# Performance work log

Hardware: AMD Instinct MI355X
Metric: run time of the kernel (lower is better)

## Reference

```python
import jax, jax.numpy as jnp
import numpy as np

# torchvision Grayscale luminance weights
_GRAY_W = np.array([0.2989, 0.587, 0.114], dtype=np.float32)

# Unnormalized DCT-II matrix as used by torch_dct.dct(norm=None):
#   X_k = 2 * sum_n x_n * cos(pi * (2n+1) * k / (2N)),  N = 8
_N = 8
_n = np.arange(_N)
_DCT_M = (2.0 * np.cos(np.pi * (2.0 * _n[None, :] + 1.0) * _n[:, None] / (2.0 * _N))).astype(np.float32)  # [k, n]


def setup_inputs() -> dict:
    key = jax.random.key(0)
    # (B, C, T, H, W) video batch in [0, 1)
    x = jax.random.uniform(key, (8, 3, 32, 256, 256), dtype=jnp.float32)
    return {"x": x}


def reference(x):
    B, C, T, H, W = x.shape
    # permute (B, C, T, H, W) -> (B, T, C, H, W)
    x = jnp.transpose(x, (0, 2, 1, 3, 4))
    # Grayscale: weighted sum over channel dim, then squeeze -> (B, T, H, W)
    gw = jnp.asarray(_GRAY_W, dtype=x.dtype)
    g = jnp.einsum('btchw,c->bthw', x, gw)
    # unfold(2,8,8).unfold(3,8,8) -> (B, T, H/8, W/8, 8, 8) non-overlapping blocks
    hb, wb = H // _N, W // _N
    blocks = g.reshape(B, T, hb, _N, wb, _N)
    blocks = jnp.transpose(blocks, (0, 1, 2, 4, 3, 5))  # (B, T, hb, wb, 8, 8)
    blocks = blocks.reshape(B, T, hb * wb, _N, _N)
    # dct_2d(norm=None): DCT-II along last dim, then along second-to-last
    # == D @ X @ D^T for each 8x8 block
    D = jnp.asarray(_DCT_M, dtype=x.dtype)
    out = jnp.einsum('kn,btpnm,lm->btpkl', D, blocks, D)
    return out
```

## Files before the change

### kernel.cpp

```cpp
#include <hip/hip_runtime.h>


#define TPB 256

__global__ __launch_bounds__(TPB) void dct_gray_kernel(
    const float* __restrict__ x, float* __restrict__ out) {
  constexpr int T = 32, H = 256, W = 256;
  __shared__ float g[8][256];
  __shared__ float Dm[64];

  const int wg  = blockIdx.x;
  const int tid = threadIdx.x;
  const int bt  = wg >> 5;
  const int hb  = wg & 31;

  if (tid < 64) {
    const int k = tid >> 3, n = tid & 7;
    Dm[tid] = 2.0f * cosf(0.19634954084936207f * (float)((2 * n + 1) * k));
  }

  const int b = bt >> 5;
  const int t = bt & 31;
  const size_t cstride = (size_t)T * H * W;
  const size_t base0 =
      ((size_t)(b * 3) * T + (size_t)t) * (size_t)(H * W) + (size_t)hb * 8 * W;

  const float w0 = 0.2989f, w1 = 0.587f, w2 = 0.114f;

#pragma unroll
  for (int i = tid; i < 512; i += TPB) {
    const int r  = i >> 6;
    const int c4 = i & 63;
    const size_t off = base0 + (size_t)r * W + (size_t)(c4 * 4);
    const float4 a = *(const float4*)(x + off);
    const float4 bb = *(const float4*)(x + off + cstride);
    const float4 cc = *(const float4*)(x + off + 2 * cstride);
    float4 gg;
    gg.x = w0 * a.x + w1 * bb.x + w2 * cc.x;
    gg.y = w0 * a.y + w1 * bb.y + w2 * cc.y;
    gg.z = w0 * a.z + w1 * bb.z + w2 * cc.z;
    gg.w = w0 * a.w + w1 * bb.w + w2 * cc.w;
    *(float4*)(&g[r][c4 * 4]) = gg;
  }
  __syncthreads();

  const int p = tid >> 3;
  const int k = tid & 7;

  float temp[8];
#pragma unroll
  for (int m = 0; m < 8; ++m) temp[m] = 0.0f;
#pragma unroll
  for (int n = 0; n < 8; ++n) {
    const float dkn = Dm[k * 8 + n];
    const float4 g0 = *(const float4*)(&g[n][p * 8]);
    const float4 g1 = *(const float4*)(&g[n][p * 8 + 4]);
    temp[0] += dkn * g0.x; temp[1] += dkn * g0.y;
    temp[2] += dkn * g0.z; temp[3] += dkn * g0.w;
    temp[4] += dkn * g1.x; temp[5] += dkn * g1.y;
    temp[6] += dkn * g1.z; temp[7] += dkn * g1.w;
  }

  float res[8];
#pragma unroll
  for (int l = 0; l < 8; ++l) {
    float acc = 0.0f;
#pragma unroll
    for (int m = 0; m < 8; ++m) acc += temp[m] * Dm[l * 8 + m];
    res[l] = acc;
  }

  float* o = out + (size_t)wg * 2048 + (size_t)tid * 8;
  *(float4*)(o)     = make_float4(res[0], res[1], res[2], res[3]);
  *(float4*)(o + 4) = make_float4(res[4], res[5], res[6], res[7]);
}

extern "C" void kernel_launch(void* const* d_in, const int* in_sizes, int n_in,
                              void* d_out, int out_size, void* d_ws, size_t ws_size,
                              hipStream_t stream) {
  const float* x = (const float*)d_in[0];
  float* out = (float*)d_out;
  dct_gray_kernel<<<8192, TPB, 0, stream>>>(x, out);
}
```

Before: 288.4 us.

## Make kernel persistent with register-prefetched double-buffered strips and constant DCT table

```diff
diff --git a/kernel.cpp b/kernel.cpp
--- a/kernel.cpp
+++ b/kernel.cpp
@@ -2,77 +2,119 @@
 
 
 #define TPB 256
+#define GRID 2048
+#define NSTRIP 8192
+
+#define DCT_TABLE { \
+  2.0f, 2.0f, 2.0f, 2.0f, 2.0f, 2.0f, 2.0f, 2.0f, \
+  1.9615705608064609f, 1.6629392246050905f, 1.1111404660392044f, 0.3901806440322565f, \
+ -0.3901806440322565f,-1.1111404660392044f,-1.6629392246050905f,-1.9615705608064609f, \
+  1.8477590650225735f, 0.7653668647301796f,-0.7653668647301796f,-1.8477590650225735f, \
+ -1.8477590650225735f,-0.7653668647301796f, 0.7653668647301796f, 1.8477590650225735f, \
+  1.6629392246050905f,-0.3901806440322565f,-1.9615705608064609f,-1.1111404660392044f, \
+  1.1111404660392044f, 1.9615705608064609f, 0.3901806440322565f,-1.6629392246050905f, \
+  1.4142135623730951f,-1.4142135623730951f,-1.4142135623730951f, 1.4142135623730951f, \
+  1.4142135623730951f,-1.4142135623730951f,-1.4142135623730951f, 1.4142135623730951f, \
+  1.1111404660392044f,-1.9615705608064609f, 0.3901806440322565f, 1.6629392246050905f, \
+ -1.6629392246050905f,-0.3901806440322565f, 1.9615705608064609f,-1.1111404660392044f, \
+  0.7653668647301796f,-1.8477590650225735f, 1.8477590650225735f,-0.7653668647301796f, \
+ -0.7653668647301796f, 1.8477590650225735f,-1.8477590650225735f, 0.7653668647301796f, \
+  0.3901806440322565f,-1.1111404660392044f, 1.6629392246050905f,-1.9615705608064609f, \
+  1.9615705608064609f,-1.6629392246050905f, 1.1111404660392044f,-0.3901806440322565f  \
+}
+
+constexpr float DCT8C[64] = DCT_TABLE;
+__device__ __constant__ float DCT8G[64] = DCT_TABLE;
 
 __global__ __launch_bounds__(TPB) void dct_gray_kernel(
     const float* __restrict__ x, float* __restrict__ out) {
   constexpr int T = 32, H = 256, W = 256;
-  __shared__ float g[8][256];
+  __shared__ float g[2][8][256];
   __shared__ float Dm[64];
 
-  const int wg  = blockIdx.x;
   const int tid = threadIdx.x;
-  const int bt  = wg >> 5;
-  const int hb  = wg & 31;
+  const int bid = blockIdx.x;
+  if (tid < 64) Dm[tid] = DCT8G[tid];
 
-  if (tid < 64) {
-    const int k = tid >> 3, n = tid & 7;
-    Dm[tid] = 2.0f * cosf(0.19634954084936207f * (float)((2 * n + 1) * k));
-  }
-
-  const int b = bt >> 5;
-  const int t = bt & 31;
   const size_t cstride = (size_t)T * H * W;
-  const size_t base0 =
-      ((size_t)(b * 3) * T + (size_t)t) * (size_t)(H * W) + (size_t)hb * 8 * W;
-
   const float w0 = 0.2989f, w1 = 0.587f, w2 = 0.114f;
 
-#pragma unroll
-  for (int i = tid; i < 512; i += TPB) {
-    const int r  = i >> 6;
-    const int c4 = i & 63;
-    const size_t off = base0 + (size_t)r * W + (size_t)(c4 * 4);
-    const float4 a = *(const float4*)(x + off);
-    const float4 bb = *(const float4*)(x + off + cstride);
-    const float4 cc = *(const float4*)(x + off + 2 * cstride);
-    float4 gg;
-    gg.x = w0 * a.x + w1 * bb.x + w2 * cc.x;
-    gg.y = w0 * a.y + w1 * bb.y + w2 * cc.y;
-    gg.z = w0 * a.z + w1 * bb.z + w2 * cc.z;
-    gg.w = w0 * a.w + w1 * bb.w + w2 * cc.w;
-    *(float4*)(&g[r][c4 * 4]) = gg;
-  }
-  __syncthreads();
+  const int r0 = tid >> 6;
+  const int c4 = tid & 63;
+  const size_t lane_off0 = (size_t)r0 * W + (size_t)(c4 * 4);
+  const size_t lane_off1 = (size_t)(r0 + 4) * W + (size_t)(c4 * 4);
 
+  float4 a[2][3];
+
+  auto issue_loads = [&](int strip) {
+    const int bt = strip >> 5, hb = strip & 31;
+    const int b = bt >> 5, t = bt & 31;
+    const size_t base0 =
+        ((size_t)(b * 3) * T + (size_t)t) * (size_t)(H * W) +
+        (size_t)hb * 8 * W;
+    const float* p0 = x + base0 + lane_off0;
+    const float* p1 = x + base0 + lane_off1;
+    a[0][0] = *(const float4*)(p0);
+    a[0][1] = *(const float4*)(p0 + cstride);
+    a[0][2] = *(const float4*)(p0 + 2 * cstride);
+    a[1][0] = *(const float4*)(p1);
+    a[1][1] = *(const float4*)(p1 + cstride);
+    a[1][2] = *(const float4*)(p1 + 2 * cstride);
+  };
+
+  issue_loads(bid);
+
+  int buf = 0;
   const int p = tid >> 3;
   const int k = tid & 7;
 
-  float temp[8];
 #pragma unroll
-  for (int m = 0; m < 8; ++m) temp[m] = 0.0f;
+  for (int j = 0; j < 4; ++j) {
+    const int s = bid + j * GRID;
+
 #pragma unroll
-  for (int n = 0; n < 8; ++n) {
-    const float dkn = Dm[k * 8 + n];
-    const float4 g0 = *(const float4*)(&g[n][p * 8]);
-    const float4 g1 = *(const float4*)(&g[n][p * 8 + 4]);
-    temp[0] += dkn * g0.x; temp[1] += dkn * g0.y;
-    temp[2] += dkn * g0.z; temp[3] += dkn * g0.w;
-    temp[4] += dkn * g1.x; temp[5] += dkn * g1.y;
-    temp[6] += dkn * g1.z; temp[7] += dkn * g1.w;
+    for (int it = 0; it < 2; ++it) {
+      float4 gg;
+      gg.x = w0 * a[it][0].x + w1 * a[it][1].x + w2 * a[it][2].x;
+      gg.y = w0 * a[it][0].y + w1 * a[it][1].y + w2 * a[it][2].y;
+      gg.z = w0 * a[it][0].z + w1 * a[it][1].z + w2 * a[it][2].z;
+      gg.w = w0 * a[it][0].w + w1 * a[it][1].w + w2 * a[it][2].w;
+      *(float4*)(&g[buf][r0 + it * 4][c4 * 4]) = gg;
+    }
+
+    if (j < 3) issue_loads(bid + (j + 1) * GRID);
+
+    __syncthreads();
+
+    float temp[8];
+#pragma unroll
+    for (int m = 0; m < 8; ++m) temp[m] = 0.0f;
+#pragma unroll
+    for (int n = 0; n < 8; ++n) {
+      const float dkn = Dm[k * 8 + n];
+      const float4 g0 = *(const float4*)(&g[buf][n][p * 8]);
+      const float4 g1 = *(const float4*)(&g[buf][n][p * 8 + 4]);
+      temp[0] += dkn * g0.x; temp[1] += dkn * g0.y;
+      temp[2] += dkn * g0.z; temp[3] += dkn * g0.w;
+      temp[4] += dkn * g1.x; temp[5] += dkn * g1.y;
+      temp[6] += dkn * g1.z; temp[7] += dkn * g1.w;
+    }
+
+    float res[8];
+#pragma unroll
+    for (int l = 0; l < 8; ++l) {
+      float acc = temp[0] * DCT8C[l * 8 + 0];
+#pragma unroll
+      for (int m = 1; m < 8; ++m) acc += temp[m] * DCT8C[l * 8 + m];
+      res[l] = acc;
+    }
+
+    float* o = out + (size_t)s * 2048 + (size_t)tid * 8;
+    *(float4*)(o)     = make_float4(res[0], res[1], res[2], res[3]);
+    *(float4*)(o + 4) = make_float4(res[4], res[5], res[6], res[7]);
+
+    buf ^= 1;
   }
-
-  float res[8];
-#pragma unroll
-  for (int l = 0; l < 8; ++l) {
-    float acc = 0.0f;
-#pragma unroll
-    for (int m = 0; m < 8; ++m) acc += temp[m] * Dm[l * 8 + m];
-    res[l] = acc;
-  }
-
-  float* o = out + (size_t)wg * 2048 + (size_t)tid * 8;
-  *(float4*)(o)     = make_float4(res[0], res[1], res[2], res[3]);
-  *(float4*)(o + 4) = make_float4(res[4], res[5], res[6], res[7]);
 }
 
 extern "C" void kernel_launch(void* const* d_in, const int* in_sizes, int n_in,
@@ -80,5 +122,5 @@
                               hipStream_t stream) {
   const float* x = (const float*)d_in[0];
   float* out = (float*)d_out;
-  dct_gray_kernel<<<8192, TPB, 0, stream>>>(x, out);
+  dct_gray_kernel<<<GRID, TPB, 0, stream>>>(x, out);
 }
```

New measurement: 292.3 us. Within noise of the previous version (+1.4%).

## Compute each 8x8 DCT block per thread in registers with butterfly row transform

Applied to the files above, without the earlier changes.

```diff
diff --git a/kernel.cpp b/kernel.cpp
--- a/kernel.cpp
+++ b/kernel.cpp
@@ -3,76 +3,115 @@
 
 #define TPB 256
 
+#define C1 1.9615705608064609f
+#define C2 1.8477590650225735f
+#define C3 1.6629392246050905f
+#define C4 1.4142135623730951f
+#define C5 1.1111404660392044f
+#define C6 0.7653668647301796f
+#define C7 0.3901806440322565f
+
+__device__ __forceinline__ constexpr float dmk(int k, int n) {
+  constexpr float DM[8][8] = {
+      {2.f, 2.f, 2.f, 2.f, 2.f, 2.f, 2.f, 2.f},
+      {C1, C3, C5, C7, -C7, -C5, -C3, -C1},
+      {C2, C6, -C6, -C2, -C2, -C6, C6, C2},
+      {C3, -C7, -C1, -C5, C5, C1, C7, -C3},
+      {C4, -C4, -C4, C4, C4, -C4, -C4, C4},
+      {C5, -C1, C7, C3, -C3, -C7, C1, -C5},
+      {C6, -C2, C2, -C6, -C6, C2, -C2, C6},
+      {C7, -C5, C3, -C1, C1, -C3, C5, -C7}};
+  return DM[k][n];
+}
+
 __global__ __launch_bounds__(TPB) void dct_gray_kernel(
     const float* __restrict__ x, float* __restrict__ out) {
-  constexpr int T = 32, H = 256, W = 256;
-  __shared__ float g[8][256];
-  __shared__ float Dm[64];
+  constexpr size_t HW = 65536;
+  constexpr size_t CS = 32 * HW;
 
-  const int wg  = blockIdx.x;
-  const int tid = threadIdx.x;
-  const int bt  = wg >> 5;
-  const int hb  = wg & 31;
+  const int n  = blockIdx.x * TPB + threadIdx.x;
+  const int s  = n >> 5;
+  const int p  = n & 31;
+  const int bt = s >> 5;
+  const int hb = s & 31;
+  const int b  = bt >> 5;
+  const int tt = bt & 31;
 
-  if (tid < 64) {
-    const int k = tid >> 3, n = tid & 7;
-    Dm[tid] = 2.0f * cosf(0.19634954084936207f * (float)((2 * n + 1) * k));
-  }
-
-  const int b = bt >> 5;
-  const int t = bt & 31;
-  const size_t cstride = (size_t)T * H * W;
-  const size_t base0 =
-      ((size_t)(b * 3) * T + (size_t)t) * (size_t)(H * W) + (size_t)hb * 8 * W;
+  const float* bp = x + ((size_t)(b * 3) * 32 + (size_t)tt) * HW +
+                    (size_t)hb * (8 * 256) + (size_t)(p * 8);
 
   const float w0 = 0.2989f, w1 = 0.587f, w2 = 0.114f;
 
-#pragma unroll
-  for (int i = tid; i < 512; i += TPB) {
-    const int r  = i >> 6;
-    const int c4 = i & 63;
-    const size_t off = base0 + (size_t)r * W + (size_t)(c4 * 4);
-    const float4 a = *(const float4*)(x + off);
-    const float4 bb = *(const float4*)(x + off + cstride);
-    const float4 cc = *(const float4*)(x + off + 2 * cstride);
-    float4 gg;
-    gg.x = w0 * a.x + w1 * bb.x + w2 * cc.x;
-    gg.y = w0 * a.y + w1 * bb.y + w2 * cc.y;
-    gg.z = w0 * a.z + w1 * bb.z + w2 * cc.z;
-    gg.w = w0 * a.w + w1 * bb.w + w2 * cc.w;
-    *(float4*)(&g[r][c4 * 4]) = gg;
-  }
-  __syncthreads();
+  float4 A0, A1, B0, B1, Cc0, Cc1;
+  float4 nA0, nA1, nB0, nB1, nC0, nC1;
 
-  const int p = tid >> 3;
-  const int k = tid & 7;
-
-  float temp[8];
-#pragma unroll
-  for (int m = 0; m < 8; ++m) temp[m] = 0.0f;
-#pragma unroll
-  for (int n = 0; n < 8; ++n) {
-    const float dkn = Dm[k * 8 + n];
-    const float4 g0 = *(const float4*)(&g[n][p * 8]);
-    const float4 g1 = *(const float4*)(&g[n][p * 8 + 4]);
-    temp[0] += dkn * g0.x; temp[1] += dkn * g0.y;
-    temp[2] += dkn * g0.z; temp[3] += dkn * g0.w;
-    temp[4] += dkn * g1.x; temp[5] += dkn * g1.y;
-    temp[6] += dkn * g1.z; temp[7] += dkn * g1.w;
+#define LOADROW(r, a0, a1, b0, b1, c0, c1)            \
+  {                                                   \
+    const float* q = bp + (size_t)(r) * 256;          \
+    a0 = *(const float4*)(q);                         \
+    a1 = *(const float4*)(q + 4);                     \
+    b0 = *(const float4*)(q + CS);                    \
+    b1 = *(const float4*)(q + CS + 4);                \
+    c0 = *(const float4*)(q + 2 * CS);                \
+    c1 = *(const float4*)(q + 2 * CS + 4);            \
   }
 
-  float res[8];
+  float o[8][8];
 #pragma unroll
-  for (int l = 0; l < 8; ++l) {
-    float acc = 0.0f;
+  for (int k = 0; k < 8; ++k)
 #pragma unroll
-    for (int m = 0; m < 8; ++m) acc += temp[m] * Dm[l * 8 + m];
-    res[l] = acc;
+    for (int l = 0; l < 8; ++l) o[k][l] = 0.0f;
+
+  LOADROW(0, A0, A1, B0, B1, Cc0, Cc1);
+
+#pragma unroll
+  for (int r = 0; r < 8; ++r) {
+    if (r < 7) LOADROW(r + 1, nA0, nA1, nB0, nB1, nC0, nC1);
+
+    float g[8];
+    g[0] = w0 * A0.x + w1 * B0.x + w2 * Cc0.x;
+    g[1] = w0 * A0.y + w1 * B0.y + w2 * Cc0.y;
+    g[2] = w0 * A0.z + w1 * B0.z + w2 * Cc0.z;
+    g[3] = w0 * A0.w + w1 * B0.w + w2 * Cc0.w;
+    g[4] = w0 * A1.x + w1 * B1.x + w2 * Cc1.x;
+    g[5] = w0 * A1.y + w1 * B1.y + w2 * Cc1.y;
+    g[6] = w0 * A1.z + w1 * B1.z + w2 * Cc1.z;
+    g[7] = w0 * A1.w + w1 * B1.w + w2 * Cc1.w;
+
+    const float e0 = g[0] + g[7], e1 = g[1] + g[6];
+    const float e2 = g[2] + g[5], e3 = g[3] + g[4];
+    const float q0 = g[0] - g[7], q1 = g[1] - g[6];
+    const float q2 = g[2] - g[5], q3 = g[3] - g[4];
+    const float ee0 = e0 + e3, ee1 = e1 + e2;
+    const float eo0 = e0 - e3, eo1 = e1 - e2;
+
+    float trow[8];
+    trow[0] = 2.0f * (ee0 + ee1);
+    trow[4] = C4 * (ee0 - ee1);
+    trow[2] = C2 * eo0 + C6 * eo1;
+    trow[6] = C6 * eo0 - C2 * eo1;
+    trow[1] = C1 * q0 + C3 * q1 + C5 * q2 + C7 * q3;
+    trow[3] = C3 * q0 - C7 * q1 - C1 * q2 - C5 * q3;
+    trow[5] = C5 * q0 - C1 * q1 + C7 * q2 + C3 * q3;
+    trow[7] = C7 * q0 - C5 * q1 + C3 * q2 - C1 * q3;
+
+#pragma unroll
+    for (int k = 0; k < 8; ++k) {
+      const float dkr = dmk(k, r);
+#pragma unroll
+      for (int l = 0; l < 8; ++l) o[k][l] += dkr * trow[l];
+    }
+
+    A0 = nA0; A1 = nA1; B0 = nB0; B1 = nB1; Cc0 = nC0; Cc1 = nC1;
   }
 
-  float* o = out + (size_t)wg * 2048 + (size_t)tid * 8;
-  *(float4*)(o)     = make_float4(res[0], res[1], res[2], res[3]);
-  *(float4*)(o + 4) = make_float4(res[4], res[5], res[6], res[7]);
+  float* op = out + (size_t)bt * 65536 + ((size_t)(hb * 32 + p)) * 64;
+#pragma unroll
+  for (int k = 0; k < 8; ++k) {
+    *(float4*)(op + k * 8)     = make_float4(o[k][0], o[k][1], o[k][2], o[k][3]);
+    *(float4*)(op + k * 8 + 4) = make_float4(o[k][4], o[k][5], o[k][6], o[k][7]);
+  }
+#undef LOADROW
 }
 
 extern "C" void kernel_launch(void* const* d_in, const int* in_sizes, int n_in,
@@ -80,5 +119,5 @@
                               hipStream_t stream) {
   const float* x = (const float*)d_in[0];
   float* out = (float*)d_out;
-  dct_gray_kernel<<<8192, TPB, 0, stream>>>(x, out);
+  dct_gray_kernel<<<1024, TPB, 0, stream>>>(x, out);
 }
```

Result: slower. 314.5 us (+9.0%).

## Compute 8x8 DCT per wavefront with butterfly factorization and lane shuffles

Applied to the files above, without the earlier changes.

```diff
diff --git a/kernel.cpp b/kernel.cpp
--- a/kernel.cpp
+++ b/kernel.cpp
@@ -3,76 +3,109 @@
 
 #define TPB 256
 
+#define C1 1.9615705608064609f
+#define C2 1.8477590650225735f
+#define C3 1.6629392246050905f
+#define C4 1.4142135623730951f
+#define C5 1.1111404660392044f
+#define C6 0.7653668647301796f
+#define C7 0.3901806440322565f
+
+__device__ __forceinline__ float4 f4add(float4 a, float4 b) {
+  return make_float4(a.x + b.x, a.y + b.y, a.z + b.z, a.w + b.w);
+}
+__device__ __forceinline__ float4 f4sub(float4 a, float4 b) {
+  return make_float4(a.x - b.x, a.y - b.y, a.z - b.z, a.w - b.w);
+}
+__device__ __forceinline__ float4 f4scale(float s, float4 a) {
+  return make_float4(s * a.x, s * a.y, s * a.z, s * a.w);
+}
+__device__ __forceinline__ float4 f4fma(float s, float4 a, float4 acc) {
+  return make_float4(fmaf(s, a.x, acc.x), fmaf(s, a.y, acc.y),
+                     fmaf(s, a.z, acc.z), fmaf(s, a.w, acc.w));
+}
+
 __global__ __launch_bounds__(TPB) void dct_gray_kernel(
     const float* __restrict__ x, float* __restrict__ out) {
-  constexpr int T = 32, H = 256, W = 256;
-  __shared__ float g[8][256];
-  __shared__ float Dm[64];
+  constexpr size_t HW = 65536;
+  constexpr size_t CS = 32 * HW;
 
-  const int wg  = blockIdx.x;
-  const int tid = threadIdx.x;
-  const int bt  = wg >> 5;
-  const int hb  = wg & 31;
+  const int wid  = blockIdx.x * (TPB / 64) + (threadIdx.x >> 6);
+  const int lane = threadIdx.x & 63;
+  const int bt = wid >> 5, hb = wid & 31;
+  const int b  = bt >> 5,  t  = bt & 31;
 
-  if (tid < 64) {
-    const int k = tid >> 3, n = tid & 7;
-    Dm[tid] = 2.0f * cosf(0.19634954084936207f * (float)((2 * n + 1) * k));
+  const float* bp = x + ((size_t)(b * 3) * 32 + (size_t)t) * HW +
+                    (size_t)hb * 2048 + (size_t)(lane * 4);
+
+  const float w0 = 0.2989f, w1 = 0.587f, w2 = 0.114f;
+  float4 G[8];
+#pragma unroll
+  for (int r = 0; r < 8; ++r) {
+    const float* q = bp + (size_t)r * 256;
+    const float4 a  = *(const float4*)(q);
+    const float4 bb = *(const float4*)(q + CS);
+    const float4 cc = *(const float4*)(q + 2 * CS);
+    G[r] = f4fma(w2, cc, f4fma(w1, bb, f4scale(w0, a)));
   }
 
-  const int b = bt >> 5;
-  const int t = bt & 31;
-  const size_t cstride = (size_t)T * H * W;
-  const size_t base0 =
-      ((size_t)(b * 3) * T + (size_t)t) * (size_t)(H * W) + (size_t)hb * 8 * W;
+  float4 tc[8];
+  {
+    const float4 e0 = f4add(G[0], G[7]), e1 = f4add(G[1], G[6]);
+    const float4 e2 = f4add(G[2], G[5]), e3 = f4add(G[3], G[4]);
+    const float4 q0 = f4sub(G[0], G[7]), q1 = f4sub(G[1], G[6]);
+    const float4 q2 = f4sub(G[2], G[5]), q3 = f4sub(G[3], G[4]);
+    const float4 ee0 = f4add(e0, e3), ee1 = f4add(e1, e2);
+    const float4 eo0 = f4sub(e0, e3), eo1 = f4sub(e1, e2);
+    tc[0] = f4scale(2.0f, f4add(ee0, ee1));
+    tc[4] = f4scale(C4, f4sub(ee0, ee1));
+    tc[2] = f4fma(C6, eo1, f4scale(C2, eo0));
+    tc[6] = f4fma(-C2, eo1, f4scale(C6, eo0));
+    tc[1] = f4fma(C7, q3, f4fma(C5, q2, f4fma(C3, q1, f4scale(C1, q0))));
+    tc[3] = f4fma(-C5, q3, f4fma(-C1, q2, f4fma(-C7, q1, f4scale(C3, q0))));
+    tc[5] = f4fma(C3, q3, f4fma(C7, q2, f4fma(-C1, q1, f4scale(C5, q0))));
+    tc[7] = f4fma(-C1, q3, f4fma(C3, q2, f4fma(-C5, q1, f4scale(C7, q0))));
+  }
 
-  const float w0 = 0.2989f, w1 = 0.587f, w2 = 0.114f;
+  float4 othr[8];
+#pragma unroll
+  for (int k = 0; k < 8; ++k) {
+    othr[k].x = __shfl_xor(tc[k].x, 1);
+    othr[k].y = __shfl_xor(tc[k].y, 1);
+    othr[k].z = __shfl_xor(tc[k].z, 1);
+    othr[k].w = __shfl_xor(tc[k].w, 1);
+  }
+
+  const int h = lane & 1;
+  float* ob = out + (size_t)bt * 65536 + (size_t)hb * 2048 +
+              (size_t)(lane >> 1) * 64 + (size_t)(h * 4);
 
 #pragma unroll
-  for (int i = tid; i < 512; i += TPB) {
-    const int r  = i >> 6;
-    const int c4 = i & 63;
-    const size_t off = base0 + (size_t)r * W + (size_t)(c4 * 4);
-    const float4 a = *(const float4*)(x + off);
-    const float4 bb = *(const float4*)(x + off + cstride);
-    const float4 cc = *(const float4*)(x + off + 2 * cstride);
-    float4 gg;
-    gg.x = w0 * a.x + w1 * bb.x + w2 * cc.x;
-    gg.y = w0 * a.y + w1 * bb.y + w2 * cc.y;
-    gg.z = w0 * a.z + w1 * bb.z + w2 * cc.z;
-    gg.w = w0 * a.w + w1 * bb.w + w2 * cc.w;
-    *(float4*)(&g[r][c4 * 4]) = gg;
+  for (int k = 0; k < 8; ++k) {
+    const float4 mine = tc[k], oth = othr[k];
+    const float v0 = h ? oth.x : mine.x, v1 = h ? oth.y : mine.y;
+    const float v2 = h ? oth.z : mine.z, v3 = h ? oth.w : mine.w;
+    const float v4 = h ? mine.x : oth.x, v5 = h ? mine.y : oth.y;
+    const float v6 = h ? mine.z : oth.z, v7 = h ? mine.w : oth.w;
+
+    const float e0 = v0 + v7, e1 = v1 + v6, e2 = v2 + v5, e3 = v3 + v4;
+    const float q0 = v0 - v7, q1 = v1 - v6, q2 = v2 - v5, q3 = v3 - v4;
+    const float ee0 = e0 + e3, ee1 = e1 + e2;
+    const float eo0 = e0 - e3, eo1 = e1 - e2;
+
+    const float t0 = 2.0f * (ee0 + ee1);
+    const float t4 = C4 * (ee0 - ee1);
+    const float t2 = C2 * eo0 + C6 * eo1;
+    const float t6 = C6 * eo0 - C2 * eo1;
+    const float t1 = C1 * q0 + C3 * q1 + C5 * q2 + C7 * q3;
+    const float t3 = C3 * q0 - C7 * q1 - C1 * q2 - C5 * q3;
+    const float t5 = C5 * q0 - C1 * q1 + C7 * q2 + C3 * q3;
+    const float t7 = C7 * q0 - C5 * q1 + C3 * q2 - C1 * q3;
+
+    const float4 res = make_float4(h ? t4 : t0, h ? t5 : t1,
+                                   h ? t6 : t2, h ? t7 : t3);
+    *(float4*)(ob + k * 8) = res;
   }
-  __syncthreads();
-
-  const int p = tid >> 3;
-  const int k = tid & 7;
-
-  float temp[8];
-#pragma unroll
-  for (int m = 0; m < 8; ++m) temp[m] = 0.0f;
-#pragma unroll
-  for (int n = 0; n < 8; ++n) {
-    const float dkn = Dm[k * 8 + n];
-    const float4 g0 = *(const float4*)(&g[n][p * 8]);
-    const float4 g1 = *(const float4*)(&g[n][p * 8 + 4]);
-    temp[0] += dkn * g0.x; temp[1] += dkn * g0.y;
-    temp[2] += dkn * g0.z; temp[3] += dkn * g0.w;
-    temp[4] += dkn * g1.x; temp[5] += dkn * g1.y;
-    temp[6] += dkn * g1.z; temp[7] += dkn * g1.w;
-  }
-
-  float res[8];
-#pragma unroll
-  for (int l = 0; l < 8; ++l) {
-    float acc = 0.0f;
-#pragma unroll
-    for (int m = 0; m < 8; ++m) acc += temp[m] * Dm[l * 8 + m];
-    res[l] = acc;
-  }
-
-  float* o = out + (size_t)wg * 2048 + (size_t)tid * 8;
-  *(float4*)(o)     = make_float4(res[0], res[1], res[2], res[3]);
-  *(float4*)(o + 4) = make_float4(res[4], res[5], res[6], res[7]);
 }
 
 extern "C" void kernel_launch(void* const* d_in, const int* in_sizes, int n_in,
@@ -80,5 +113,5 @@
                               hipStream_t stream) {
   const float* x = (const float*)d_in[0];
   float* out = (float*)d_out;
-  dct_gray_kernel<<<8192, TPB, 0, stream>>>(x, out);
+  dct_gray_kernel<<<2048, TPB, 0, stream>>>(x, out);
 }
```

New measurement: 292.6 us. Within noise of the previous version (+1.5%).
